# Optimization experiments

Measured on AMD Instinct MI355X. Metric: run time of the kernel, lower is better.

Reference implementation:

```python
import jax, jax.numpy as jnp
import numpy as np

H, W = 30, 30
D = 256
MAX_OBJECTS = 16
SENT = H * W  # sentinel label for background / invalid slots


def label_components(grid):
    """4-connected same-color connected-component labeling.
    grid: [B,H,W] int32. Returns labels [B,H,W] where each foreground cell
    carries the minimum linear index of its component (== raster-scan BFS
    discovery order of the torch code), SENT for background."""
    B = grid.shape[0]
    lin = jnp.arange(H * W, dtype=jnp.int32).reshape(1, H, W)
    fg = grid > 0
    init = jnp.where(fg, lin, SENT).astype(jnp.int32)
    big = jnp.int32(SENT)

    def nbr_min(lab):
        lp = jnp.pad(lab, ((0, 0), (1, 1), (1, 1)), constant_values=SENT)
        gp = jnp.pad(grid, ((0, 0), (1, 1), (1, 1)), constant_values=-1)
        m = lab
        for di, dj in ((-1, 0), (1, 0), (0, -1), (0, 1)):
            ls = lp[:, 1 + di:1 + di + H, 1 + dj:1 + dj + W]
            gs = gp[:, 1 + di:1 + di + H, 1 + dj:1 + dj + W]
            m = jnp.minimum(m, jnp.where(gs == grid, ls, big))
        return jnp.where(fg, m, big)

    def cond(s):
        return s[1]

    def body(s):
        lab, _ = s
        new = nbr_min(lab)
        # pointer jumping: label <- min(label, label[label]) accelerates convergence
        flat = new.reshape(B, H * W)
        jumped = jnp.take_along_axis(flat, jnp.clip(flat, 0, H * W - 1), axis=1)
        flat = jnp.where(flat < SENT, jnp.minimum(flat, jumped), SENT)
        new = flat.reshape(B, H, W)
        return new, jnp.any(new != lab)

    labels, _ = jax.lax.while_loop(cond, body, (init, jnp.array(True)))
    return labels


def extract_objects(grid, labels):
    """Per-slot (color, y, x, h, w, valid), each [B, MAX_OBJECTS]."""
    B = grid.shape[0]
    HW = H * W
    lin = jnp.arange(HW, dtype=jnp.int32)
    rows, cols = lin // W, lin % W
    lab = labels.reshape(B, HW)
    ns = HW + 1  # extra segment collects background
    seg = jnp.where(lab < SENT, lab, SENT)
    rmin = jax.vmap(lambda s: jax.ops.segment_min(rows, s, num_segments=ns))(seg)
    rmax = jax.vmap(lambda s: jax.ops.segment_max(rows, s, num_segments=ns))(seg)
    cmin = jax.vmap(lambda s: jax.ops.segment_min(cols, s, num_segments=ns))(seg)
    cmax = jax.vmap(lambda s: jax.ops.segment_max(cols, s, num_segments=ns))(seg)
    # component roots, in raster order == BFS discovery order; keep first K
    root = jnp.where((lab == lin[None, :]) & (lab < SENT), lin[None, :], SENT)
    order = jnp.sort(root, axis=1)[:, :MAX_OBJECTS]
    valid = order < SENT
    idx = jnp.clip(order, 0, HW - 1)
    bi = jnp.arange(B)[:, None]
    y = jnp.clip(rmin[bi, idx], 0, H - 1)
    x = jnp.clip(cmin[bi, idx], 0, W - 1)
    y2 = jnp.clip(rmax[bi, idx] + 1, y + 1, H)
    x2 = jnp.clip(cmax[bi, idx] + 1, x + 1, W)
    color = grid.reshape(B, HW)[bi, idx]
    return color, y, x, y2 - y, x2 - x, valid


def forward(grid_emb, structure_rep, W1, b1, W2, b2, Wp, bp, gamma, beta, ortho_scale, objs):
    color, y, x, h, w, valid = objs
    B = grid_emb.shape[0]
    bi = jnp.arange(B)[:, None]
    # summed-area table -> bbox mean-pool of grid_emb in O(1) per object
    S = jnp.pad(jnp.cumsum(jnp.cumsum(grid_emb, axis=1), axis=2),
                ((0, 0), (1, 0), (1, 0), (0, 0)))
    y2, x2 = y + h, x + w
    pool = S[bi, y2, x2] - S[bi, y, x2] - S[bi, y2, x] + S[bi, y, x]
    pool = pool / (h * w).astype(grid_emb.dtype)[..., None]       # [B,K,D]
    bbox = jnp.stack([color / 9.0, x / W, y / H, w / W, h / H], axis=-1).astype(grid_emb.dtype)
    combined = jnp.concatenate([pool, bbox], axis=-1)              # [B,K,D+5]
    hdn = jax.nn.gelu(jnp.einsum('bkf,fd->bkd', combined, W1) + b1, approximate=False)
    obj = jnp.einsum('bkd,de->bke', hdn, W2) + b2
    obj = jnp.where(valid[..., None], obj, 0.0)  # pad slots are zero embeddings
    # OrthogonalProjector with structure broadcast = mean over structure slots
    s = structure_rep.mean(axis=1, keepdims=True)                  # [B,1,D]
    sn = s / jnp.maximum(jnp.linalg.norm(s, axis=-1, keepdims=True), 1e-8)
    dot = (obj * sn).sum(axis=-1, keepdims=True)
    co = (obj - dot * sn) * ortho_scale
    co = jnp.einsum('bkd,de->bke', co, Wp) + bp
    mu = co.mean(axis=-1, keepdims=True)
    var = ((co - mu) ** 2).mean(axis=-1, keepdims=True)
    return (co - mu) / jnp.sqrt(var + 1e-5) * gamma + beta


def setup_inputs() -> dict:
    key = jax.random.key(0)
    ks = jax.random.split(key, 6)
    B, K_STRUCT = 128, 8
    grid_emb = jax.random.normal(ks[0], (B, H, W, D), dtype=jnp.float32)
    grid = jax.random.randint(ks[1], (B, H, W), 0, 10, dtype=jnp.int32)
    structure_rep = jax.random.normal(ks[2], (B, K_STRUCT, D), dtype=jnp.float32)
    sc = 0.02
    W1 = jax.random.normal(ks[3], (D + 5, D), dtype=jnp.float32) * sc
    b1 = jnp.zeros((D,), jnp.float32)
    W2 = jax.random.normal(ks[4], (D, D), dtype=jnp.float32) * sc
    b2 = jnp.zeros((D,), jnp.float32)
    Wp = jax.random.normal(ks[5], (D, D), dtype=jnp.float32) * sc
    bp = jnp.zeros((D,), jnp.float32)
    gamma = jnp.ones((D,), jnp.float32)
    beta = jnp.zeros((D,), jnp.float32)
    ortho_scale = jnp.ones((1,), jnp.float32)
    return dict(grid_emb=grid_emb, grid=grid, structure_rep=structure_rep,
                W1=W1, b1=b1, W2=W2, b2=b2, Wp=Wp, bp=bp,
                gamma=gamma, beta=beta, ortho_scale=ortho_scale)


def reference(grid_emb, grid, structure_rep, W1, b1, W2, b2, Wp, bp, gamma, beta, ortho_scale):
    labels = label_components(grid)
    objs = extract_objects(grid, labels)
    return forward(grid_emb, structure_rep, W1, b1, W2, b2, Wp, bp, gamma, beta, ortho_scale, objs)
```

## Files before the change

### kernel.cpp

```cpp
#include <hip/hip_runtime.h>
#include <math.h>

#define HH 30
#define WWID 30
#define HW 900
#define SENTV 900
#define DD 256
#define MAXK 16
#define A_LD 264

#define COMP(v, jj) ((jj) == 0 ? (v).x : (jj) == 1 ? (v).y : (jj) == 2 ? (v).z : (v).w)

__device__ __forceinline__ float gelu_exact(float x) {
    return 0.5f * x * (1.0f + erff(x * 0.70710678118654752440f));
}

__device__ __forceinline__ void gemm_phase(
    const float (* __restrict__ Asrc)[A_LD],
    const float* __restrict__ Wm,
    float (* __restrict__ part)[8][DD],
    int wv, int c0)
{
    const int kbase = wv * 32;
    float acc[8][4];
    #pragma unroll
    for (int r = 0; r < 8; ++r) { acc[r][0] = 0.f; acc[r][1] = 0.f; acc[r][2] = 0.f; acc[r][3] = 0.f; }

    const float* wp = Wm + (size_t)kbase * DD + c0;
    float4 wc[8], wn[8];
    #pragma unroll
    for (int j = 0; j < 8; ++j) wc[j] = *(const float4*)(wp + (size_t)j * DD);

    #pragma unroll
    for (int ch = 0; ch < 4; ++ch) {
        if (ch < 3) {
            const float* wpn = wp + (size_t)((ch + 1) * 8) * DD;
            #pragma unroll
            for (int j = 0; j < 8; ++j) wn[j] = *(const float4*)(wpn + (size_t)j * DD);
        }
        float4 aA[8], aB[8];
        #pragma unroll
        for (int r = 0; r < 8; ++r) {
            aA[r] = *(const float4*)(&Asrc[r][kbase + ch * 8]);
            aB[r] = *(const float4*)(&Asrc[r][kbase + ch * 8 + 4]);
        }
        #pragma unroll
        for (int j = 0; j < 4; ++j) {
            #pragma unroll
            for (int r = 0; r < 8; ++r) {
                float av = COMP(aA[r], j);
                acc[r][0] += av * wc[j].x;
                acc[r][1] += av * wc[j].y;
                acc[r][2] += av * wc[j].z;
                acc[r][3] += av * wc[j].w;
            }
        }
        #pragma unroll
        for (int j = 0; j < 4; ++j) {
            #pragma unroll
            for (int r = 0; r < 8; ++r) {
                float av = COMP(aB[r], j);
                acc[r][0] += av * wc[4 + j].x;
                acc[r][1] += av * wc[4 + j].y;
                acc[r][2] += av * wc[4 + j].z;
                acc[r][3] += av * wc[4 + j].w;
            }
        }
        if (ch < 3) {
            #pragma unroll
            for (int j = 0; j < 8; ++j) wc[j] = wn[j];
        }
    }

    #pragma unroll
    for (int r = 0; r < 8; ++r)
        *(float4*)(&part[wv][r][c0]) = make_float4(acc[r][0], acc[r][1], acc[r][2], acc[r][3]);
    __syncthreads();
}

#define REDUCE8(sv)                                                           \
    float4 sv = *(const float4*)(&part_s[0][wv][c0]);                         \
    {                                                                         \
        _Pragma("unroll")                                                     \
        for (int w = 1; w < 8; ++w) {                                         \
            float4 p = *(const float4*)(&part_s[w][wv][c0]);                  \
            sv.x += p.x; sv.y += p.y; sv.z += p.z; sv.w += p.w;               \
        }                                                                     \
    }

__global__ __launch_bounds__(512, 2) void ccce_fused(
    const float* __restrict__ grid_emb,
    const int* __restrict__ grid,
    const float* __restrict__ structure_rep,
    const float* __restrict__ W1, const float* __restrict__ b1,
    const float* __restrict__ W2, const float* __restrict__ b2,
    const float* __restrict__ Wp, const float* __restrict__ bp,
    const float* __restrict__ gvec, const float* __restrict__ bvec,
    const float* __restrict__ ortho_scale,
    float* __restrict__ out, int KS)
{
    const int b   = blockIdx.x >> 1;
    const int h8  = blockIdx.x & 1;
    const int tid = threadIdx.x;
    const int tx  = tid & 63;
    const int wv  = tid >> 6;
    const int c0  = tx * 4;

    __shared__ int color_s[HW];
    __shared__ int lab_s[HW];
    __shared__ int slot_of[HW];
    __shared__ int root_s[MAXK];
    __shared__ int nroot_s;
    __shared__ int by0[MAXK], by1[MAXK], bx0[MAXK], bx1[MAXK];
    __shared__ __align__(16) float A1_s[8][A_LD];
    __shared__ __align__(16) float A2_s[8][A_LD];
    __shared__ __align__(16) float part_s[8][8][DD];
    __shared__ __align__(16) float sn_s[DD];
    __shared__ float red_s[4];

    const int4* gp = (const int4*)(grid + (size_t)b * HW);
    int4 g;
    if (tid < 225) g = gp[tid];

    const bool do_s = (tid < DD);
    float sl0 = 0.f, sl1 = 0.f, sl2 = 0.f, sl3 = 0.f, sl4 = 0.f, sl5 = 0.f, sl6 = 0.f, sl7 = 0.f;
    float s_gen = 0.f;
    {
        const float* sr = structure_rep + (size_t)b * KS * DD + tid;
        if (do_s) {
            if (KS == 8) {
                sl0 = sr[0 * DD]; sl1 = sr[1 * DD]; sl2 = sr[2 * DD]; sl3 = sr[3 * DD];
                sl4 = sr[4 * DD]; sl5 = sr[5 * DD]; sl6 = sr[6 * DD]; sl7 = sr[7 * DD];
            } else {
                for (int j = 0; j < KS; ++j) s_gen += sr[(size_t)j * DD];
            }
        }
    }

    if (tid < 225) {
        int i = tid * 4;
        color_s[i + 0] = g.x; lab_s[i + 0] = (g.x > 0) ? (i + 0) : SENTV;
        color_s[i + 1] = g.y; lab_s[i + 1] = (g.y > 0) ? (i + 1) : SENTV;
        color_s[i + 2] = g.z; lab_s[i + 2] = (g.z > 0) ? (i + 2) : SENTV;
        color_s[i + 3] = g.w; lab_s[i + 3] = (g.w > 0) ? (i + 3) : SENTV;
    }
    __syncthreads();

    const int li0 = tid;
    const int li1 = tid + 512;
    int nm0 = 0, nm1 = 0;
    {
        int c = color_s[li0];
        if (c > 0) {
            int r = li0 / WWID, cc = li0 - (li0 / WWID) * WWID;
            nm0 = 16;
            if (r > 0        && color_s[li0 - WWID] == c) nm0 |= 1;
            if (r < HH - 1   && color_s[li0 + WWID] == c) nm0 |= 2;
            if (cc > 0       && color_s[li0 - 1]    == c) nm0 |= 4;
            if (cc < WWID-1  && color_s[li0 + 1]    == c) nm0 |= 8;
        }
    }
    if (li1 < HW) {
        int c = color_s[li1];
        if (c > 0) {
            int r = li1 / WWID, cc = li1 - (li1 / WWID) * WWID;
            nm1 = 16;
            if (r > 0        && color_s[li1 - WWID] == c) nm1 |= 1;
            if (r < HH - 1   && color_s[li1 + WWID] == c) nm1 |= 2;
            if (cc > 0       && color_s[li1 - 1]    == c) nm1 |= 4;
            if (cc < WWID-1  && color_s[li1 + 1]    == c) nm1 |= 8;
        }
    }

    for (;;) {
        int ch = 0;
        int m0 = 0, m1 = 0;
        if (nm0 & 16) {
            m0 = lab_s[li0];
            if (nm0 & 1) m0 = min(m0, lab_s[li0 - WWID]);
            if (nm0 & 2) m0 = min(m0, lab_s[li0 + WWID]);
            if (nm0 & 4) m0 = min(m0, lab_s[li0 - 1]);
            if (nm0 & 8) m0 = min(m0, lab_s[li0 + 1]);
        }
        if (nm1 & 16) {
            m1 = lab_s[li1];
            if (nm1 & 1) m1 = min(m1, lab_s[li1 - WWID]);
            if (nm1 & 2) m1 = min(m1, lab_s[li1 + WWID]);
            if (nm1 & 4) m1 = min(m1, lab_s[li1 - 1]);
            if (nm1 & 8) m1 = min(m1, lab_s[li1 + 1]);
        }
        if (nm0 & 16) m0 = min(m0, lab_s[m0]);
        if (nm1 & 16) m1 = min(m1, lab_s[m1]);
        if (nm0 & 16) m0 = min(m0, lab_s[m0]);
        if (nm1 & 16) m1 = min(m1, lab_s[m1]);
        if ((nm0 & 16) && m0 < lab_s[li0]) { lab_s[li0] = m0; ch = 1; }
        if ((nm1 & 16) && m1 < lab_s[li1]) { lab_s[li1] = m1; ch = 1; }
        if (__syncthreads_count(ch) == 0) break;
    }

    if (tid < 64) {
        int base = 0;
        for (int chk = 0; chk < 15; ++chk) {
            int cell = chk * 64 + tid;
            bool isr = (cell < HW) && (color_s[cell] > 0) && (lab_s[cell] == cell);
            unsigned long long mask = __ballot(isr);
            int rank = base + __popcll(mask & ((1ull << tid) - 1ull));
            if (isr && rank < MAXK) root_s[rank] = cell;
            base += __popcll(mask);
        }
        if (tid == 0) nroot_s = base;
    } else {
        for (int i = tid - 64; i < HW; i += 448) slot_of[i] = -1;
        if (tid >= 448 && tid < 448 + MAXK) {
            int k = tid - 448;
            by0[k] = HH; by1[k] = -1; bx0[k] = WWID; bx1[k] = -1;
        }
    }
    __syncthreads();

    const int nval = min(nroot_s, MAXK);
    if (tid < nval) slot_of[root_s[tid]] = tid;
    __syncthreads();

    if (nm0 & 16) {
        int s = slot_of[lab_s[li0]];
        if (s >= 0) {
            int r = li0 / WWID, cc = li0 - (li0 / WWID) * WWID;
            atomicMin(&by0[s], r); atomicMax(&by1[s], r);
            atomicMin(&bx0[s], cc); atomicMax(&bx1[s], cc);
        }
    }
    if (nm1 & 16) {
        int s = slot_of[lab_s[li1]];
        if (s >= 0) {
            int r = li1 / WWID, cc = li1 - (li1 / WWID) * WWID;
            atomicMin(&by0[s], r); atomicMax(&by1[s], r);
            atomicMin(&bx0[s], cc); atomicMax(&bx1[s], cc);
        }
    }

    float s_mean = (KS == 8)
        ? (sl0 + sl1 + sl2 + sl3 + sl4 + sl5 + sl6 + sl7) * 0.125f
        : s_gen * (1.0f / (float)KS);
    {
        float ss = s_mean * s_mean;
        #pragma unroll
        for (int off = 32; off > 0; off >>= 1) ss += __shfl_xor(ss, off);
        if (tx == 0 && wv < 4) red_s[wv] = ss;
    }
    __syncthreads();

    if (do_s) {
        float nrm = sqrtf(red_s[0] + red_s[1] + red_s[2] + red_s[3]);
        sn_s[tid] = s_mean / fmaxf(nrm, 1e-8f);
    }
    const int slot = h8 * 8 + wv;
    const int v_ok = (slot < nval) ? 1 : 0;
    {
        float4 pv = make_float4(0.f, 0.f, 0.f, 0.f);
        int y = 0, x = 0, h = 1, w = 1, col = 0;
        if (v_ok) {
            y = by0[slot]; x = bx0[slot];
            h = by1[slot] + 1 - y; w = bx1[slot] + 1 - x;
            col = color_s[root_s[slot]];
            const int n = h * w;
            const float* bp_ = grid_emb + ((size_t)(b * HH + y) * WWID + x) * DD + c0;
            float4 sum = make_float4(0.f, 0.f, 0.f, 0.f);
            for (int base = 0; base < n; base += 8) {
                float4 v[8];
                #pragma unroll
                for (int t = 0; t < 8; ++t) {
                    int ii = base + t;
                    if (ii < n) {
                        int yy = ii / w, xx = ii - yy * w;
                        v[t] = *(const float4*)(bp_ + ((size_t)yy * WWID + xx) * DD);
                    }
                }
                #pragma unroll
                for (int t = 0; t < 8; ++t) {
                    int ii = base + t;
                    if (ii < n) { sum.x += v[t].x; sum.y += v[t].y; sum.z += v[t].z; sum.w += v[t].w; }
                }
            }
            float inv = 1.0f / (float)n;
            pv.x = sum.x * inv; pv.y = sum.y * inv; pv.z = sum.z * inv; pv.w = sum.w * inv;
        }
        *(float4*)(&A1_s[wv][c0]) = pv;
        if (tx < 8) {
            float f = 0.f;
            if (v_ok && tx < 5) {
                switch (tx) {
                    case 0: f = (float)col / 9.0f; break;
                    case 1: f = (float)x  / 30.0f; break;
                    case 2: f = (float)y  / 30.0f; break;
                    case 3: f = (float)w  / 30.0f; break;
                    case 4: f = (float)h  / 30.0f; break;
                }
            }
            A1_s[wv][256 + tx] = f;
        }
    }
    __syncthreads();

    gemm_phase(A1_s, W1, part_s, wv, c0);
    {
        REDUCE8(s);
        #pragma unroll
        for (int j = 0; j < 5; ++j) {
            float a = A1_s[wv][256 + j];
            float4 wrow = *(const float4*)(W1 + (size_t)(256 + j) * DD + c0);
            s.x += a * wrow.x; s.y += a * wrow.y; s.z += a * wrow.z; s.w += a * wrow.w;
        }
        float4 bb = *(const float4*)(b1 + c0);
        float4 hv;
        hv.x = gelu_exact(s.x + bb.x);
        hv.y = gelu_exact(s.y + bb.y);
        hv.z = gelu_exact(s.z + bb.z);
        hv.w = gelu_exact(s.w + bb.w);
        *(float4*)(&A2_s[wv][c0]) = hv;
    }
    __syncthreads();

    gemm_phase(A2_s, W2, part_s, wv, c0);
    {
        REDUCE8(s);
        float4 bb = *(const float4*)(b2 + c0);
        float vm = v_ok ? 1.f : 0.f;
        float o0 = (s.x + bb.x) * vm;
        float o1 = (s.y + bb.y) * vm;
        float o2 = (s.z + bb.z) * vm;
        float o3 = (s.w + bb.w) * vm;
        float4 snv = *(const float4*)(sn_s + c0);
        float p = o0 * snv.x + o1 * snv.y + o2 * snv.z + o3 * snv.w;
        #pragma unroll
        for (int off = 32; off > 0; off >>= 1) p += __shfl_xor(p, off);
        float osc = ortho_scale[0];
        float4 co;
        co.x = (o0 - p * snv.x) * osc;
        co.y = (o1 - p * snv.y) * osc;
        co.z = (o2 - p * snv.z) * osc;
        co.w = (o3 - p * snv.w) * osc;
        *(float4*)(&A1_s[wv][c0]) = co;
    }
    __syncthreads();

    gemm_phase(A1_s, Wp, part_s, wv, c0);
    {
        REDUCE8(s);
        float4 bb = *(const float4*)(bp + c0);
        float v0 = s.x + bb.x;
        float v1 = s.y + bb.y;
        float v2 = s.z + bb.z;
        float v3 = s.w + bb.w;
        float sm = v0 + v1 + v2 + v3;
        float sq = v0 * v0 + v1 * v1 + v2 * v2 + v3 * v3;
        #pragma unroll
        for (int off = 32; off > 0; off >>= 1) {
            sm += __shfl_xor(sm, off);
            sq += __shfl_xor(sq, off);
        }
        float mu   = sm * (1.0f / 256.0f);
        float var  = fmaxf(sq * (1.0f / 256.0f) - mu * mu, 0.0f);
        float rstd = 1.0f / sqrtf(var + 1e-5f);
        float4 gv = *(const float4*)(gvec + c0);
        float4 bv = *(const float4*)(bvec + c0);
        float4 o;
        o.x = (v0 - mu) * rstd * gv.x + bv.x;
        o.y = (v1 - mu) * rstd * gv.y + bv.y;
        o.z = (v2 - mu) * rstd * gv.z + bv.z;
        o.w = (v3 - mu) * rstd * gv.w + bv.w;
        *(float4*)(out + ((size_t)b * MAXK + slot) * DD + c0) = o;
    }
}

extern "C" void kernel_launch(void* const* d_in, const int* in_sizes, int n_in,
                              void* d_out, int out_size, void* d_ws, size_t ws_size,
                              hipStream_t stream) {
    const float* grid_emb = (const float*)d_in[0];
    const int*   grid     = (const int*)d_in[1];
    const float* srep     = (const float*)d_in[2];
    const float* W1v = (const float*)d_in[3];
    const float* b1v = (const float*)d_in[4];
    const float* W2v = (const float*)d_in[5];
    const float* b2v = (const float*)d_in[6];
    const float* Wpv = (const float*)d_in[7];
    const float* bpv = (const float*)d_in[8];
    const float* gv  = (const float*)d_in[9];
    const float* bv  = (const float*)d_in[10];
    const float* osv = (const float*)d_in[11];
    float* out = (float*)d_out;

    const int B  = in_sizes[1] / HW;
    const int KS = in_sizes[2] / (B * DD);

    hipLaunchKernelGGL(ccce_fused, dim3(B * 2), dim3(512), 0, stream,
                       grid_emb, grid, srep, W1v, b1v, W2v, b2v, Wpv, bpv,
                       gv, bv, osv, out, KS);
}
```

Baseline: 28.49 us.

## Replace FP32 split-K GEMMs with bf16 MFMA using pre-swizzled weights

Adds a pre-pass kernel that converts W1, W2 and Wp to bf16 in a fragment-swizzled layout in the workspace each call. The main kernel then runs the three 256x256 MLP stages on 16x16x32 bf16 MFMA instructions, with A tiles held as bf16 in shared memory. This removes the FP32 FMA split-K loop and its 64KB partial-sum reduction buffer. The cost is an extra kernel launch, reduced precision from bf16 inputs, and extra cross-wave reductions for the projection and layernorm.

```diff
diff --git a/kernel.cpp b/kernel.cpp
--- a/kernel.cpp
+++ b/kernel.cpp
@@ -7,94 +7,71 @@
 #define SENTV 900
 #define DD 256
 #define MAXK 16
-#define A_LD 264
-
-#define COMP(v, jj) ((jj) == 0 ? (v).x : (jj) == 1 ? (v).y : (jj) == 2 ? (v).z : (v).w)
+#define AK 264
+
+typedef __attribute__((ext_vector_type(8))) short short8b;
+typedef __attribute__((ext_vector_type(4))) float f32x4;
 
 __device__ __forceinline__ float gelu_exact(float x) {
     return 0.5f * x * (1.0f + erff(x * 0.70710678118654752440f));
 }
 
-__device__ __forceinline__ void gemm_phase(
-    const float (* __restrict__ Asrc)[A_LD],
-    const float* __restrict__ Wm,
-    float (* __restrict__ part)[8][DD],
-    int wv, int c0)
+__device__ __forceinline__ unsigned short f2bf(float x) {
+    unsigned int u = __float_as_uint(x);
+    u += 0x7FFFu + ((u >> 16) & 1u);
+    return (unsigned short)(u >> 16);
+}
+
+__global__ __launch_bounds__(256) void conv_w(
+    const float* __restrict__ W1, const float* __restrict__ W2,
+    const float* __restrict__ Wp, unsigned short* __restrict__ ws)
 {
-    const int kbase = wv * 32;
-    float acc[8][4];
+    int f = blockIdx.x * 256 + threadIdx.x;
+    int m = f >> 13;
+    int rem = f & 8191;
+    int ntile = rem >> 9;
+    int kl = rem & 511;
+    int ktile = kl >> 6;
+    int lane = kl & 63;
+    const float* W = (m == 0) ? W1 : (m == 1) ? W2 : Wp;
+    int k0 = ktile * 32 + (lane >> 4) * 8;
+    int n  = ntile * 16 + (lane & 15);
+    unsigned short* dst = ws + (size_t)m * 65536 +
+                          ((size_t)(ntile * 8 + ktile) * 64 + lane) * 8;
     #pragma unroll
-    for (int r = 0; r < 8; ++r) { acc[r][0] = 0.f; acc[r][1] = 0.f; acc[r][2] = 0.f; acc[r][3] = 0.f; }
-
-    const float* wp = Wm + (size_t)kbase * DD + c0;
-    float4 wc[8], wn[8];
+    for (int i = 0; i < 8; ++i) dst[i] = f2bf(W[(size_t)(k0 + i) * DD + n]);
+}
+
+__device__ __forceinline__ void mfma_pass(
+    const unsigned short (* __restrict__ ab)[AK],
+    const unsigned short* __restrict__ wm,
+    f32x4 acc[2], int cl, int tx, int wv)
+{
+    short8b afr[8];
     #pragma unroll
-    for (int j = 0; j < 8; ++j) wc[j] = *(const float4*)(wp + (size_t)j * DD);
-
+    for (int kt = 0; kt < 8; ++kt)
+        afr[kt] = *(const short8b*)&ab[cl][kt * 32 + (tx >> 4) * 8];
+    const short8b* base = (const short8b*)wm;
     #pragma unroll
-    for (int ch = 0; ch < 4; ++ch) {
-        if (ch < 3) {
-            const float* wpn = wp + (size_t)((ch + 1) * 8) * DD;
-            #pragma unroll
-            for (int j = 0; j < 8; ++j) wn[j] = *(const float4*)(wpn + (size_t)j * DD);
-        }
-        float4 aA[8], aB[8];
+    for (int t = 0; t < 2; ++t) {
+        const int nt = wv * 2 + t;
+        short8b bfr[8];
         #pragma unroll
-        for (int r = 0; r < 8; ++r) {
-            aA[r] = *(const float4*)(&Asrc[r][kbase + ch * 8]);
-            aB[r] = *(const float4*)(&Asrc[r][kbase + ch * 8 + 4]);
-        }
+        for (int kt = 0; kt < 8; ++kt)
+            bfr[kt] = base[(nt * 8 + kt) * 64 + tx];
         #pragma unroll
-        for (int j = 0; j < 4; ++j) {
-            #pragma unroll
-            for (int r = 0; r < 8; ++r) {
-                float av = COMP(aA[r], j);
-                acc[r][0] += av * wc[j].x;
-                acc[r][1] += av * wc[j].y;
-                acc[r][2] += av * wc[j].z;
-                acc[r][3] += av * wc[j].w;
-            }
-        }
-        #pragma unroll
-        for (int j = 0; j < 4; ++j) {
-            #pragma unroll
-            for (int r = 0; r < 8; ++r) {
-                float av = COMP(aB[r], j);
-                acc[r][0] += av * wc[4 + j].x;
-                acc[r][1] += av * wc[4 + j].y;
-                acc[r][2] += av * wc[4 + j].z;
-                acc[r][3] += av * wc[4 + j].w;
-            }
-        }
-        if (ch < 3) {
-            #pragma unroll
-            for (int j = 0; j < 8; ++j) wc[j] = wn[j];
-        }
-    }
-
-    #pragma unroll
-    for (int r = 0; r < 8; ++r)
-        *(float4*)(&part[wv][r][c0]) = make_float4(acc[r][0], acc[r][1], acc[r][2], acc[r][3]);
-    __syncthreads();
-}
-
-#define REDUCE8(sv)                                                           \
-    float4 sv = *(const float4*)(&part_s[0][wv][c0]);                         \
-    {                                                                         \
-        _Pragma("unroll")                                                     \
-        for (int w = 1; w < 8; ++w) {                                         \
-            float4 p = *(const float4*)(&part_s[w][wv][c0]);                  \
-            sv.x += p.x; sv.y += p.y; sv.z += p.z; sv.w += p.w;               \
-        }                                                                     \
-    }
-
-__global__ __launch_bounds__(512, 2) void ccce_fused(
+        for (int kt = 0; kt < 8; ++kt)
+            acc[t] = __builtin_amdgcn_mfma_f32_16x16x32_bf16(afr[kt], bfr[kt], acc[t], 0, 0, 0);
+    }
+}
+
+__global__ __launch_bounds__(512, 2) void ccce_main(
     const float* __restrict__ grid_emb,
     const int* __restrict__ grid,
     const float* __restrict__ structure_rep,
+    const unsigned short* __restrict__ wsw,
     const float* __restrict__ W1, const float* __restrict__ b1,
-    const float* __restrict__ W2, const float* __restrict__ b2,
-    const float* __restrict__ Wp, const float* __restrict__ bp,
+    const float* __restrict__ b2, const float* __restrict__ bp,
     const float* __restrict__ gvec, const float* __restrict__ bvec,
     const float* __restrict__ ortho_scale,
     float* __restrict__ out, int KS)
@@ -104,7 +81,8 @@
     const int tid = threadIdx.x;
     const int tx  = tid & 63;
     const int wv  = tid >> 6;
-    const int c0  = tx * 4;
+    const int cl  = tx & 15;
+    const int g   = tx >> 4;
 
     __shared__ int color_s[HW];
     __shared__ int lab_s[HW];
@@ -112,25 +90,31 @@
     __shared__ int root_s[MAXK];
     __shared__ int nroot_s;
     __shared__ int by0[MAXK], by1[MAXK], bx0[MAXK], bx1[MAXK];
-    __shared__ __align__(16) float A1_s[8][A_LD];
-    __shared__ __align__(16) float A2_s[8][A_LD];
-    __shared__ __align__(16) float part_s[8][8][DD];
+    __shared__ __align__(16) unsigned short a0[16][AK];
+    __shared__ __align__(16) unsigned short a1[16][AK];
     __shared__ __align__(16) float sn_s[DD];
     __shared__ float red_s[4];
+    __shared__ float feats_s[8][5];
+    __shared__ float dred[8][8];
+    __shared__ float lred[8][8][2];
+
+    for (int i = tid; i < 16 * AK; i += 512) {
+        ((unsigned short*)a0)[i] = 0;
+        ((unsigned short*)a1)[i] = 0;
+    }
 
     const int4* gp = (const int4*)(grid + (size_t)b * HW);
-    int4 g;
-    if (tid < 225) g = gp[tid];
+    int4 gld;
+    if (tid < 225) gld = gp[tid];
 
     const bool do_s = (tid < DD);
-    float sl0 = 0.f, sl1 = 0.f, sl2 = 0.f, sl3 = 0.f, sl4 = 0.f, sl5 = 0.f, sl6 = 0.f, sl7 = 0.f;
-    float s_gen = 0.f;
+    float sl0=0.f,sl1=0.f,sl2=0.f,sl3=0.f,sl4=0.f,sl5=0.f,sl6=0.f,sl7=0.f,s_gen=0.f;
     {
         const float* sr = structure_rep + (size_t)b * KS * DD + tid;
         if (do_s) {
             if (KS == 8) {
-                sl0 = sr[0 * DD]; sl1 = sr[1 * DD]; sl2 = sr[2 * DD]; sl3 = sr[3 * DD];
-                sl4 = sr[4 * DD]; sl5 = sr[5 * DD]; sl6 = sr[6 * DD]; sl7 = sr[7 * DD];
+                sl0 = sr[0*DD]; sl1 = sr[1*DD]; sl2 = sr[2*DD]; sl3 = sr[3*DD];
+                sl4 = sr[4*DD]; sl5 = sr[5*DD]; sl6 = sr[6*DD]; sl7 = sr[7*DD];
             } else {
                 for (int j = 0; j < KS; ++j) s_gen += sr[(size_t)j * DD];
             }
@@ -139,25 +123,24 @@
 
     if (tid < 225) {
         int i = tid * 4;
-        color_s[i + 0] = g.x; lab_s[i + 0] = (g.x > 0) ? (i + 0) : SENTV;
-        color_s[i + 1] = g.y; lab_s[i + 1] = (g.y > 0) ? (i + 1) : SENTV;
-        color_s[i + 2] = g.z; lab_s[i + 2] = (g.z > 0) ? (i + 2) : SENTV;
-        color_s[i + 3] = g.w; lab_s[i + 3] = (g.w > 0) ? (i + 3) : SENTV;
+        color_s[i+0] = gld.x; lab_s[i+0] = (gld.x > 0) ? (i+0) : SENTV;
+        color_s[i+1] = gld.y; lab_s[i+1] = (gld.y > 0) ? (i+1) : SENTV;
+        color_s[i+2] = gld.z; lab_s[i+2] = (gld.z > 0) ? (i+2) : SENTV;
+        color_s[i+3] = gld.w; lab_s[i+3] = (gld.w > 0) ? (i+3) : SENTV;
     }
     __syncthreads();
 
-    const int li0 = tid;
-    const int li1 = tid + 512;
+    const int li0 = tid, li1 = tid + 512;
     int nm0 = 0, nm1 = 0;
     {
         int c = color_s[li0];
         if (c > 0) {
             int r = li0 / WWID, cc = li0 - (li0 / WWID) * WWID;
             nm0 = 16;
-            if (r > 0        && color_s[li0 - WWID] == c) nm0 |= 1;
-            if (r < HH - 1   && color_s[li0 + WWID] == c) nm0 |= 2;
-            if (cc > 0       && color_s[li0 - 1]    == c) nm0 |= 4;
-            if (cc < WWID-1  && color_s[li0 + 1]    == c) nm0 |= 8;
+            if (r > 0       && color_s[li0 - WWID] == c) nm0 |= 1;
+            if (r < HH - 1  && color_s[li0 + WWID] == c) nm0 |= 2;
+            if (cc > 0      && color_s[li0 - 1]    == c) nm0 |= 4;
+            if (cc < WWID-1 && color_s[li0 + 1]    == c) nm0 |= 8;
         }
     }
     if (li1 < HW) {
@@ -165,10 +148,10 @@
         if (c > 0) {
             int r = li1 / WWID, cc = li1 - (li1 / WWID) * WWID;
             nm1 = 16;
-            if (r > 0        && color_s[li1 - WWID] == c) nm1 |= 1;
-            if (r < HH - 1   && color_s[li1 + WWID] == c) nm1 |= 2;
-            if (cc > 0       && color_s[li1 - 1]    == c) nm1 |= 4;
-            if (cc < WWID-1  && color_s[li1 + 1]    == c) nm1 |= 8;
+            if (r > 0       && color_s[li1 - WWID] == c) nm1 |= 1;
+            if (r < HH - 1  && color_s[li1 + WWID] == c) nm1 |= 2;
+            if (cc > 0      && color_s[li1 - 1]    == c) nm1 |= 4;
+            if (cc < WWID-1 && color_s[li1 + 1]    == c) nm1 |= 8;
         }
     }
 
@@ -254,9 +237,11 @@
         float nrm = sqrtf(red_s[0] + red_s[1] + red_s[2] + red_s[3]);
         sn_s[tid] = s_mean / fmaxf(nrm, 1e-8f);
     }
-    const int slot = h8 * 8 + wv;
-    const int v_ok = (slot < nval) ? 1 : 0;
-    {
+
+    {
+        const int slot = h8 * 8 + wv;
+        const int v_ok = (slot < nval) ? 1 : 0;
+        const int c0 = tx * 4;
         float4 pv = make_float4(0.f, 0.f, 0.f, 0.f);
         int y = 0, x = 0, h = 1, w = 1, col = 0;
         if (v_ok) {
@@ -266,11 +251,11 @@
             const int n = h * w;
             const float* bp_ = grid_emb + ((size_t)(b * HH + y) * WWID + x) * DD + c0;
             float4 sum = make_float4(0.f, 0.f, 0.f, 0.f);
-            for (int base = 0; base < n; base += 8) {
+            for (int base2 = 0; base2 < n; base2 += 8) {
                 float4 v[8];
                 #pragma unroll
                 for (int t = 0; t < 8; ++t) {
-                    int ii = base + t;
+                    int ii = base2 + t;
                     if (ii < n) {
                         int yy = ii / w, xx = ii - yy * w;
                         v[t] = *(const float4*)(bp_ + ((size_t)yy * WWID + xx) * DD);
@@ -278,17 +263,20 @@
                 }
                 #pragma unroll
                 for (int t = 0; t < 8; ++t) {
-                    int ii = base + t;
+                    int ii = base2 + t;
                     if (ii < n) { sum.x += v[t].x; sum.y += v[t].y; sum.z += v[t].z; sum.w += v[t].w; }
                 }
             }
             float inv = 1.0f / (float)n;
             pv.x = sum.x * inv; pv.y = sum.y * inv; pv.z = sum.z * inv; pv.w = sum.w * inv;
         }
-        *(float4*)(&A1_s[wv][c0]) = pv;
-        if (tx < 8) {
+        unsigned int p0 = (unsigned int)f2bf(pv.x) | ((unsigned int)f2bf(pv.y) << 16);
+        unsigned int p1 = (unsigned int)f2bf(pv.z) | ((unsigned int)f2bf(pv.w) << 16);
+        *(unsigned int*)&a0[wv][c0]     = p0;
+        *(unsigned int*)&a0[wv][c0 + 2] = p1;
+        if (tx < 5) {
             float f = 0.f;
-            if (v_ok && tx < 5) {
+            if (v_ok) {
                 switch (tx) {
                     case 0: f = (float)col / 9.0f; break;
                     case 1: f = (float)x  / 30.0f; break;
@@ -297,79 +285,135 @@
                     case 4: f = (float)h  / 30.0f; break;
                 }
             }
-            A1_s[wv][256 + tx] = f;
+            feats_s[wv][tx] = f;
         }
     }
     __syncthreads();
 
-    gemm_phase(A1_s, W1, part_s, wv, c0);
-    {
-        REDUCE8(s);
-        #pragma unroll
-        for (int j = 0; j < 5; ++j) {
-            float a = A1_s[wv][256 + j];
-            float4 wrow = *(const float4*)(W1 + (size_t)(256 + j) * DD + c0);
-            s.x += a * wrow.x; s.y += a * wrow.y; s.z += a * wrow.z; s.w += a * wrow.w;
-        }
-        float4 bb = *(const float4*)(b1 + c0);
-        float4 hv;
-        hv.x = gelu_exact(s.x + bb.x);
-        hv.y = gelu_exact(s.y + bb.y);
-        hv.z = gelu_exact(s.z + bb.z);
-        hv.w = gelu_exact(s.w + bb.w);
-        *(float4*)(&A2_s[wv][c0]) = hv;
-    }
-    __syncthreads();
-
-    gemm_phase(A2_s, W2, part_s, wv, c0);
-    {
-        REDUCE8(s);
-        float4 bb = *(const float4*)(b2 + c0);
-        float vm = v_ok ? 1.f : 0.f;
-        float o0 = (s.x + bb.x) * vm;
-        float o1 = (s.y + bb.y) * vm;
-        float o2 = (s.z + bb.z) * vm;
-        float o3 = (s.w + bb.w) * vm;
-        float4 snv = *(const float4*)(sn_s + c0);
-        float p = o0 * snv.x + o1 * snv.y + o2 * snv.z + o3 * snv.w;
-        #pragma unroll
-        for (int off = 32; off > 0; off >>= 1) p += __shfl_xor(p, off);
-        float osc = ortho_scale[0];
-        float4 co;
-        co.x = (o0 - p * snv.x) * osc;
-        co.y = (o1 - p * snv.y) * osc;
-        co.z = (o2 - p * snv.z) * osc;
-        co.w = (o3 - p * snv.w) * osc;
-        *(float4*)(&A1_s[wv][c0]) = co;
-    }
-    __syncthreads();
-
-    gemm_phase(A1_s, Wp, part_s, wv, c0);
-    {
-        REDUCE8(s);
-        float4 bb = *(const float4*)(bp + c0);
-        float v0 = s.x + bb.x;
-        float v1 = s.y + bb.y;
-        float v2 = s.z + bb.z;
-        float v3 = s.w + bb.w;
-        float sm = v0 + v1 + v2 + v3;
-        float sq = v0 * v0 + v1 * v1 + v2 * v2 + v3 * v3;
-        #pragma unroll
-        for (int off = 32; off > 0; off >>= 1) {
-            sm += __shfl_xor(sm, off);
-            sq += __shfl_xor(sq, off);
-        }
-        float mu   = sm * (1.0f / 256.0f);
-        float var  = fmaxf(sq * (1.0f / 256.0f) - mu * mu, 0.0f);
-        float rstd = 1.0f / sqrtf(var + 1e-5f);
-        float4 gv = *(const float4*)(gvec + c0);
-        float4 bv = *(const float4*)(bvec + c0);
-        float4 o;
-        o.x = (v0 - mu) * rstd * gv.x + bv.x;
-        o.y = (v1 - mu) * rstd * gv.y + bv.y;
-        o.z = (v2 - mu) * rstd * gv.z + bv.z;
-        o.w = (v3 - mu) * rstd * gv.w + bv.w;
-        *(float4*)(out + ((size_t)b * MAXK + slot) * DD + c0) = o;
+    {
+        f32x4 acc[2] = {{0,0,0,0},{0,0,0,0}};
+        mfma_pass(a0, wsw, acc, cl, tx, wv);
+        if (g < 2) {
+            #pragma unroll
+            for (int t = 0; t < 2; ++t) {
+                int col = (wv * 2 + t) * 16 + cl;
+                float b1v = b1[col];
+                float tw[5];
+                #pragma unroll
+                for (int jj = 0; jj < 5; ++jj) tw[jj] = W1[(size_t)(256 + jj) * DD + col];
+                #pragma unroll
+                for (int j = 0; j < 4; ++j) {
+                    int row = g * 4 + j;
+                    float s = acc[t][j] + b1v;
+                    #pragma unroll
+                    for (int jj = 0; jj < 5; ++jj) s += feats_s[row][jj] * tw[jj];
+                    a1[row][col] = f2bf(gelu_exact(s));
+                }
+            }
+        }
+        __syncthreads();
+    }
+
+    {
+        f32x4 acc[2] = {{0,0,0,0},{0,0,0,0}};
+        mfma_pass(a1, wsw + 65536, acc, cl, tx, wv);
+        float obj[2][4], snc[2];
+        if (g < 2) {
+            float pd[4] = {0.f, 0.f, 0.f, 0.f};
+            #pragma unroll
+            for (int t = 0; t < 2; ++t) {
+                int col = (wv * 2 + t) * 16 + cl;
+                float b2v = b2[col];
+                snc[t] = sn_s[col];
+                #pragma unroll
+                for (int j = 0; j < 4; ++j) {
+                    int row = g * 4 + j;
+                    float vm = ((h8 * 8 + row) < nval) ? 1.f : 0.f;
+                    obj[t][j] = (acc[t][j] + b2v) * vm;
+                    pd[j] += obj[t][j] * snc[t];
+                }
+            }
+            #pragma unroll
+            for (int off = 1; off < 16; off <<= 1) {
+                #pragma unroll
+                for (int j = 0; j < 4; ++j) pd[j] += __shfl_xor(pd[j], off);
+            }
+            if (cl == 0) {
+                #pragma unroll
+                for (int j = 0; j < 4; ++j) dred[wv][g * 4 + j] = pd[j];
+            }
+        }
+        __syncthreads();
+        if (g < 2) {
+            float osc = ortho_scale[0];
+            #pragma unroll
+            for (int j = 0; j < 4; ++j) {
+                int row = g * 4 + j;
+                float p = 0.f;
+                #pragma unroll
+                for (int w = 0; w < 8; ++w) p += dred[w][row];
+                #pragma unroll
+                for (int t = 0; t < 2; ++t) {
+                    int col = (wv * 2 + t) * 16 + cl;
+                    a0[row][col] = f2bf((obj[t][j] - p * snc[t]) * osc);
+                }
+            }
+        }
+        __syncthreads();
+    }
+
+    {
+        f32x4 acc[2] = {{0,0,0,0},{0,0,0,0}};
+        mfma_pass(a0, wsw + 2 * 65536, acc, cl, tx, wv);
+        float v[2][4];
+        if (g < 2) {
+            float S[4] = {0,0,0,0}, Q[4] = {0,0,0,0};
+            #pragma unroll
+            for (int t = 0; t < 2; ++t) {
+                int col = (wv * 2 + t) * 16 + cl;
+                float bpv = bp[col];
+                #pragma unroll
+                for (int j = 0; j < 4; ++j) {
+                    v[t][j] = acc[t][j] + bpv;
+                    S[j] += v[t][j];
+                    Q[j] += v[t][j] * v[t][j];
+                }
+            }
+            #pragma unroll
+            for (int off = 1; off < 16; off <<= 1) {
+                #pragma unroll
+                for (int j = 0; j < 4; ++j) {
+                    S[j] += __shfl_xor(S[j], off);
+                    Q[j] += __shfl_xor(Q[j], off);
+                }
+            }
+            if (cl == 0) {
+                #pragma unroll
+                for (int j = 0; j < 4; ++j) {
+                    lred[wv][g * 4 + j][0] = S[j];
+                    lred[wv][g * 4 + j][1] = Q[j];
+                }
+            }
+        }
+        __syncthreads();
+        if (g < 2) {
+            #pragma unroll
+            for (int j = 0; j < 4; ++j) {
+                int row = g * 4 + j;
+                float Ss = 0.f, Qq = 0.f;
+                #pragma unroll
+                for (int w = 0; w < 8; ++w) { Ss += lred[w][row][0]; Qq += lred[w][row][1]; }
+                float mu   = Ss * (1.0f / 256.0f);
+                float var  = fmaxf(Qq * (1.0f / 256.0f) - mu * mu, 0.0f);
+                float rstd = 1.0f / sqrtf(var + 1e-5f);
+                #pragma unroll
+                for (int t = 0; t < 2; ++t) {
+                    int col = (wv * 2 + t) * 16 + cl;
+                    float o = (v[t][j] - mu) * rstd * gvec[col] + bvec[col];
+                    out[((size_t)(b * MAXK + h8 * 8 + row)) * DD + col] = o;
+                }
+            }
+        }
     }
 }
 
@@ -393,7 +437,10 @@
     const int B  = in_sizes[1] / HW;
     const int KS = in_sizes[2] / (B * DD);
 
-    hipLaunchKernelGGL(ccce_fused, dim3(B * 2), dim3(512), 0, stream,
-                       grid_emb, grid, srep, W1v, b1v, W2v, b2v, Wpv, bpv,
+    unsigned short* wsw = (unsigned short*)d_ws;
+    hipLaunchKernelGGL(conv_w, dim3(96), dim3(256), 0, stream,
+                       W1v, W2v, Wpv, wsw);
+    hipLaunchKernelGGL(ccce_main, dim3(B * 2), dim3(512), 0, stream,
+                       grid_emb, grid, srep, wsw, W1v, b1v, b2v, bpv,
                        gv, bv, osv, out, KS);
 }
```

New measurement: 28.85 us. About the same (+1.3%).
